# Performance work log

Measured on AMD Instinct MI355X. Metric: run time of the kernel, lower is better.

Reference implementation:

```python
import jax, jax.numpy as jnp
import numpy as np

H = 8      # heads
D = 64     # dim_head
N0 = 1024  # modality-0 tokens
N1 = 1024  # modality-1 tokens
N = N0 + N1  # == token_num
DI = H * D   # dim_inner = 512


def setup_inputs() -> dict:
    key = jax.random.key(0)
    ks = jax.random.split(key, 10)
    s = 0.02
    return {
        "x0": jax.random.normal(ks[0], (1, N0, 512), jnp.float32),
        "x1": jax.random.normal(ks[1], (1, N1, 512), jnp.float32),
        "mask0": jnp.ones((1, N0), jnp.bool_),
        "mask1": jnp.ones((1, N1), jnp.bool_),
        "attn_dist": jax.random.normal(ks[2], (1, N, N), jnp.float32),
        "W_in0": jax.random.normal(ks[3], (512, 3 * DI), jnp.float32) * s,
        "W_in1": jax.random.normal(ks[4], (512, 3 * DI), jnp.float32) * s,
        "W_tau": jax.random.normal(ks[5], (DI, N * H), jnp.float32) * s,
        "b_tau": jax.random.normal(ks[6], (N * H,), jnp.float32) * s,
        "W_out0": jax.random.normal(ks[7], (DI, 512), jnp.float32) * s,
        "W_out1": jax.random.normal(ks[8], (DI, 512), jnp.float32) * s,
    }


def _split_heads(qkv, B, n):
    # (B, n, 3*H*D) -> (3, B, H, n, D)   [matches Rearrange 'b n (qkv h d) -> qkv b h n d']
    return qkv.reshape(B, n, 3, H, D).transpose(2, 0, 3, 1, 4)


def reference(x0, x1, mask0, mask1, attn_dist, W_in0, W_in1, W_tau, b_tau, W_out0, W_out1):
    B = x0.shape[0]
    qkv0 = _split_heads(x0 @ W_in0, B, N0)
    qkv1 = _split_heads(x1 @ W_in1, B, N1)
    qkv = jnp.concatenate([qkv0, qkv1], axis=3)  # pack along token axis -> (3,B,H,N,D)
    q, k, v = qkv[0], qkv[1], qkv[2]
    mask = jnp.concatenate([mask0, mask1], axis=1)  # (B, N)

    sim = jnp.einsum('bhid,bhjd->bhij', q, k) / jnp.sqrt(jnp.array(D, q.dtype))
    neg = -jnp.finfo(sim.dtype).max
    sim = jnp.where(mask[:, None, None, :], sim, neg)

    # taus: raw row-major reshape of q (B,H,N,D) -> (B,N,H*D), as in torch .reshape
    q_flat = q.reshape(B, N, H * D)
    taus = (q_flat @ W_tau + b_tau).reshape(B, N, N, H)
    bias = (taus * attn_dist[..., None]).transpose(0, 3, 1, 2)  # (B,H,N,N)
    sim = sim - bias

    attn = jax.nn.softmax(sim.astype(jnp.float32), axis=-1).astype(sim.dtype)
    out = jnp.einsum('bhij,bhjd->bhid', attn, v)
    out = out.transpose(0, 2, 1, 3).reshape(B, N, H * D)  # merge heads

    out0 = out[:, :N0] @ W_out0
    out1 = out[:, N0:] @ W_out1
    return (out0, out1)
```

## Files before the change

kernel.cpp:

```cpp
#include <hip/hip_runtime.h>
#include <stdint.h>

typedef __bf16 bf16;
typedef __bf16 bf16x8 __attribute__((ext_vector_type(8)));
typedef float f32x4 __attribute__((ext_vector_type(4)));
typedef unsigned short u16x8 __attribute__((ext_vector_type(8)));

#define MFMA16(a, b, c) __builtin_amdgcn_mfma_f32_16x16x32_bf16(a, b, c, 0, 0, 0)

static __device__ __forceinline__ bf16x8 lds_frag(const unsigned short* p) {
  return __builtin_bit_cast(bf16x8, *(const u16x8*)p);
}

static __device__ __forceinline__ u16x8 cvt8(const float* p) {
  f32x4 a = *(const f32x4*)p;
  f32x4 b = *(const f32x4*)(p + 4);
  u16x8 r;
#pragma unroll
  for (int e = 0; e < 4; ++e) {
    r[e] = __builtin_bit_cast(unsigned short, (bf16)a[e]);
    r[4 + e] = __builtin_bit_cast(unsigned short, (bf16)b[e]);
  }
  return r;
}

__global__ __launch_bounds__(256) void wtau_transpose(
    const float* __restrict__ Wti, const float* __restrict__ btau,
    bf16* __restrict__ Wto, float* __restrict__ bto) {
  const int c0 = blockIdx.x * 64;
  const int j0 = blockIdx.y * 32;
  const int tid = threadIdx.x;
  __shared__ unsigned short tile[8 * 32 * 72];

#pragma unroll
  for (int it = 0; it < 8; ++it) {
    int idx = it * 256 + tid;
    int c = idx >> 5, j = idx & 31;
    u16x8 v = cvt8(Wti + (size_t)(c0 + c) * 16384 + (j0 + j) * 8);
#pragma unroll
    for (int h = 0; h < 8; ++h) tile[(h * 32 + j) * 72 + c] = v[h];
  }
  __syncthreads();
#pragma unroll
  for (int it = 0; it < 8; ++it) {
    int chunk = it * 256 + tid;
    int row = chunk >> 3, ck = chunk & 7;
    int h = row >> 5, j = row & 31;
    u16x8 v = *(const u16x8*)&tile[row * 72 + ck * 8];
    *(u16x8*)((unsigned short*)Wto + (size_t)(h * 2048 + j0 + j) * 512 + c0 + ck * 8) = v;
  }
  if (blockIdx.x == 0) {
    int idx = tid;
    int j = idx >> 3, h = idx & 7;
    bto[h * 2048 + j0 + j] = btau[(j0 + j) * 8 + h];
  }
}

__global__ __launch_bounds__(256) void qkv_gemm(
    const float* __restrict__ x0, const float* __restrict__ x1,
    const float* __restrict__ Win0, const float* __restrict__ Win1,
    bf16* __restrict__ Qb, bf16* __restrict__ Kb, bf16* __restrict__ Vb) {
  const int mod = blockIdx.z;
  const float* Am = mod ? x1 : x0;
  const float* Bm = mod ? Win1 : Win0;
  const int i0 = blockIdx.x * 64;
  const int c0 = blockIdx.y * 64;
  const int tid = threadIdx.x;
  const int lane = tid & 63, wave = tid >> 6;
  const int l16 = lane & 15, quad = lane >> 4;
  const int mrow = (wave & 1) * 32, ncol = (wave >> 1) * 32;
  __shared__ unsigned short As[64 * 32];
  __shared__ unsigned short Bs[64 * 32];
  f32x4 acc[2][2] = {};

  const int arow = tid >> 2, akc = tid & 3;
  const int bkr = tid >> 3, bnc = tid & 7;
  for (int k0 = 0; k0 < 512; k0 += 32) {
    u16x8 va = cvt8(Am + (size_t)(i0 + arow) * 512 + k0 + akc * 8);
    u16x8 vb = cvt8(Bm + (size_t)(k0 + bkr) * 1536 + c0 + bnc * 8);
    __syncthreads();
    *(u16x8*)&As[arow * 32 + akc * 8] = va;
#pragma unroll
    for (int e = 0; e < 8; ++e) Bs[(bnc * 8 + e) * 32 + bkr] = vb[e];
    __syncthreads();
    bf16x8 a[2], b[2];
#pragma unroll
    for (int mt = 0; mt < 2; ++mt) a[mt] = lds_frag(&As[(mrow + mt * 16 + l16) * 32 + quad * 8]);
#pragma unroll
    for (int nt = 0; nt < 2; ++nt) b[nt] = lds_frag(&Bs[(ncol + nt * 16 + l16) * 32 + quad * 8]);
#pragma unroll
    for (int mt = 0; mt < 2; ++mt)
#pragma unroll
      for (int nt = 0; nt < 2; ++nt) acc[mt][nt] = MFMA16(a[mt], b[nt], acc[mt][nt]);
  }
#pragma unroll
  for (int mt = 0; mt < 2; ++mt)
#pragma unroll
    for (int nt = 0; nt < 2; ++nt)
#pragma unroll
      for (int r = 0; r < 4; ++r) {
        int row = i0 + mrow + mt * 16 + quad * 4 + r;
        int col = c0 + ncol + nt * 16 + l16;
        int qsel = col >> 9, h = (col >> 6) & 7, d = col & 63;
        bf16* dst = qsel == 0 ? Qb : (qsel == 1 ? Kb : Vb);
        dst[(size_t)(h * 2048 + mod * 1024 + row) * 64 + d] = (bf16)acc[mt][nt][r];
      }
}

__global__ __launch_bounds__(256) void tau_gemm(
    const bf16* __restrict__ Qb, const bf16* __restrict__ Wt,
    const float* __restrict__ bt, const float* __restrict__ ad, bf16* __restrict__ T) {
  const int h = blockIdx.z;
  const int i0 = blockIdx.x * 128, j0 = blockIdx.y * 128;
  const bf16* Bm = Wt + (size_t)h * (2048 * 512);
  const int tid = threadIdx.x;
  const int lane = tid & 63, wave = tid >> 6;
  const int l16 = lane & 15, quad = lane >> 4;
  const int mrow = (wave & 1) * 64, ncol = (wave >> 1) * 64;
  __shared__ unsigned short As[128 * 64];
  __shared__ unsigned short Bs[128 * 64];
  f32x4 acc[4][4] = {};

  for (int k0 = 0; k0 < 512; k0 += 64) {
    __syncthreads();
#pragma unroll
    for (int c = 0; c < 4; ++c) {
      int s = c * 256 + tid;
      int row = s >> 3, pos = s & 7;
      int kc = pos ^ (row & 7);
      __builtin_amdgcn_global_load_lds((const unsigned int*)(Qb + (size_t)(i0 + row) * 512 + k0 + kc * 8),
                                       (unsigned int*)&As[s * 8], 16, 0, 0);
      __builtin_amdgcn_global_load_lds((const unsigned int*)(Bm + (size_t)(j0 + row) * 512 + k0 + kc * 8),
                                       (unsigned int*)&Bs[s * 8], 16, 0, 0);
    }
    __syncthreads();
#pragma unroll
    for (int kb = 0; kb < 2; ++kb) {
      bf16x8 a[4], b[4];
#pragma unroll
      for (int mt = 0; mt < 4; ++mt) {
        int row = mrow + mt * 16 + l16;
        a[mt] = lds_frag(&As[row * 64 + (((kb * 4 + quad) ^ (row & 7)) * 8)]);
      }
#pragma unroll
      for (int nt = 0; nt < 4; ++nt) {
        int row = ncol + nt * 16 + l16;
        b[nt] = lds_frag(&Bs[row * 64 + (((kb * 4 + quad) ^ (row & 7)) * 8)]);
      }
#pragma unroll
      for (int mt = 0; mt < 4; ++mt)
#pragma unroll
        for (int nt = 0; nt < 4; ++nt) acc[mt][nt] = MFMA16(a[mt], b[nt], acc[mt][nt]);
    }
  }
  float btv[4];
#pragma unroll
  for (int nt = 0; nt < 4; ++nt) btv[nt] = bt[h * 2048 + j0 + ncol + nt * 16 + l16];
  bf16* Th = T + (size_t)h * (2048 * 2048);
#pragma unroll
  for (int mt = 0; mt < 4; ++mt)
#pragma unroll
    for (int nt = 0; nt < 4; ++nt)
#pragma unroll
      for (int r = 0; r < 4; ++r) {
        int row = i0 + mrow + mt * 16 + quad * 4 + r;
        int col = j0 + ncol + nt * 16 + l16;
        float av = ad[(size_t)row * 2048 + col];
        Th[(size_t)row * 2048 + col] = (bf16)((acc[mt][nt][r] + btv[nt]) * av);
      }
}

__global__ __launch_bounds__(256) void attn_kernel(
    const bf16* __restrict__ Qb, const bf16* __restrict__ Kb, const bf16* __restrict__ Vb,
    const bf16* __restrict__ T, float* __restrict__ Op, float* __restrict__ Ml) {
  const int h = blockIdx.y;
  const int i0 = blockIdx.x * 64;
  const int js = blockIdx.z;
  const int tid = threadIdx.x;
  const int lane = tid & 63, wave = tid >> 6;
  const int l16 = lane & 15, quad = lane >> 4;
  __shared__ unsigned short Ks[64 * 72];
  __shared__ unsigned short Vt[64 * 72];
  __shared__ unsigned short Ps[64 * 72];
  __shared__ unsigned short Tb[64 * 64];

  bf16x8 aQ[2];
#pragma unroll
  for (int kk = 0; kk < 2; ++kk)
    aQ[kk] = __builtin_bit_cast(
        bf16x8, *(const u16x8*)((const unsigned short*)Qb +
                                (size_t)(h * 2048 + i0 + wave * 16 + l16) * 64 + kk * 32 + quad * 8));
  f32x4 Oacc[4] = {};
  float m_run[4], l_run[4];
#pragma unroll
  for (int r = 0; r < 4; ++r) { m_run[r] = -3.0e38f; l_run[r] = 0.f; }
  const bf16* Th = T + (size_t)h * (2048 * 2048);

  for (int t = 0; t < 8; ++t) {
    const int j0 = js * 512 + t * 64;
    u16x8 vk[2], vv[2];
#pragma unroll
    for (int c = 0; c < 2; ++c) {
      int s = c * 256 + tid;
      int row = s >> 3, dc = s & 7;
      vk[c] = *(const u16x8*)((const unsigned short*)Kb + (size_t)(h * 2048 + j0 + row) * 64 + dc * 8);
      vv[c] = *(const u16x8*)((const unsigned short*)Vb + (size_t)(h * 2048 + j0 + row) * 64 + dc * 8);
    }
    __syncthreads();
#pragma unroll
    for (int c = 0; c < 2; ++c) {
      int s = c * 256 + tid;
      __builtin_amdgcn_global_load_lds(
          (const unsigned int*)(Th + (size_t)(i0 + (s >> 3)) * 2048 + j0 + (s & 7) * 8),
          (unsigned int*)&Tb[s * 8], 16, 0, 0);
      int row = s >> 3, dc = s & 7;
      *(u16x8*)&Ks[row * 72 + dc * 8] = vk[c];
#pragma unroll
      for (int e = 0; e < 8; ++e) Vt[(dc * 8 + e) * 72 + row] = vv[c][e];
    }
    __syncthreads();

    f32x4 S[4] = {};
#pragma unroll
    for (int nt = 0; nt < 4; ++nt)
#pragma unroll
      for (int kk = 0; kk < 2; ++kk) {
        bf16x8 bk = lds_frag(&Ks[(nt * 16 + l16) * 72 + kk * 32 + quad * 8]);
        S[nt] = MFMA16(aQ[kk], bk, S[nt]);
      }
    float sv[4][4];
#pragma unroll
    for (int nt = 0; nt < 4; ++nt)
#pragma unroll
      for (int r = 0; r < 4; ++r) {
        float tb = (float)__builtin_bit_cast(
            bf16, Tb[(wave * 16 + quad * 4 + r) * 64 + nt * 16 + l16]);
        sv[nt][r] = S[nt][r] * 0.125f - tb;
      }
#pragma unroll
    for (int r = 0; r < 4; ++r) {
      float mx = fmaxf(fmaxf(sv[0][r], sv[1][r]), fmaxf(sv[2][r], sv[3][r]));
#pragma unroll
      for (int o = 1; o < 16; o <<= 1) mx = fmaxf(mx, __shfl_xor(mx, o, 16));
      float mnew = fmaxf(m_run[r], mx);
      float alpha = __expf(m_run[r] - mnew);
      m_run[r] = mnew;
      float rs = 0.f;
#pragma unroll
      for (int nt = 0; nt < 4; ++nt) { sv[nt][r] = __expf(sv[nt][r] - mnew); rs += sv[nt][r]; }
#pragma unroll
      for (int o = 1; o < 16; o <<= 1) rs += __shfl_xor(rs, o, 16);
      l_run[r] = l_run[r] * alpha + rs;
#pragma unroll
      for (int dt = 0; dt < 4; ++dt) Oacc[dt][r] *= alpha;
    }
#pragma unroll
    for (int nt = 0; nt < 4; ++nt)
#pragma unroll
      for (int r = 0; r < 4; ++r)
        Ps[(wave * 16 + quad * 4 + r) * 72 + nt * 16 + l16] =
            __builtin_bit_cast(unsigned short, (bf16)sv[nt][r]);
    __syncthreads();
#pragma unroll
    for (int kk = 0; kk < 2; ++kk) {
      bf16x8 aP = lds_frag(&Ps[(wave * 16 + l16) * 72 + kk * 32 + quad * 8]);
#pragma unroll
      for (int dt = 0; dt < 4; ++dt) {
        bf16x8 bv = lds_frag(&Vt[(dt * 16 + l16) * 72 + kk * 32 + quad * 8]);
        Oacc[dt] = MFMA16(aP, bv, Oacc[dt]);
      }
    }
  }
  const size_t pb = ((size_t)js * 8 + h) * 2048;
#pragma unroll
  for (int r = 0; r < 4; ++r) {
    int rowg = i0 + wave * 16 + quad * 4 + r;
#pragma unroll
    for (int dt = 0; dt < 4; ++dt)
      Op[(pb + rowg) * 64 + dt * 16 + l16] = Oacc[dt][r];
    if (l16 == 0) {
      Ml[(pb + rowg) * 2 + 0] = m_run[r];
      Ml[(pb + rowg) * 2 + 1] = l_run[r];
    }
  }
}

__global__ __launch_bounds__(256) void merge_kernel(
    const float* __restrict__ Op, const float* __restrict__ Ml, bf16* __restrict__ om) {
  const int gr = blockIdx.x * 4 + (threadIdx.x >> 6);
  const int d = threadIdx.x & 63;
  float ms[4];
  float mmax = -3.0e38f;
#pragma unroll
  for (int s = 0; s < 4; ++s) {
    ms[s] = Ml[((size_t)s * 16384 + gr) * 2 + 0];
    mmax = fmaxf(mmax, ms[s]);
  }
  float lsum = 0.f, o = 0.f;
#pragma unroll
  for (int s = 0; s < 4; ++s) {
    float w = __expf(ms[s] - mmax);
    lsum += Ml[((size_t)s * 16384 + gr) * 2 + 1] * w;
    o += Op[((size_t)s * 16384 + gr) * 64 + d] * w;
  }
  int h = gr >> 11, i = gr & 2047;
  om[(size_t)i * 512 + h * 64 + d] = (bf16)(o / lsum);
}

__global__ __launch_bounds__(256) void out_proj(
    const bf16* __restrict__ om, const float* __restrict__ Wo0, const float* __restrict__ Wo1,
    float* __restrict__ out) {
  const int mod = blockIdx.z;
  const bf16* Am = om + (size_t)mod * (1024 * 512);
  const float* Bm = mod ? Wo1 : Wo0;
  float* outp = out + (size_t)mod * (1024 * 512);
  const int i0 = blockIdx.x * 64;
  const int c0 = blockIdx.y * 64;
  const int tid = threadIdx.x;
  const int lane = tid & 63, wave = tid >> 6;
  const int l16 = lane & 15, quad = lane >> 4;
  const int mrow = (wave & 1) * 32, ncol = (wave >> 1) * 32;
  __shared__ unsigned short As[64 * 32];
  __shared__ unsigned short Bs[64 * 32];
  f32x4 acc[2][2] = {};

  const int arow = tid >> 2, akc = tid & 3;
  const int bkr = tid >> 3, bnc = tid & 7;
  for (int k0 = 0; k0 < 512; k0 += 32) {
    u16x8 va = *(const u16x8*)((const unsigned short*)Am + (size_t)(i0 + arow) * 512 + k0 + akc * 8);
    u16x8 vb = cvt8(Bm + (size_t)(k0 + bkr) * 512 + c0 + bnc * 8);
    __syncthreads();
    *(u16x8*)&As[arow * 32 + akc * 8] = va;
#pragma unroll
    for (int e = 0; e < 8; ++e) Bs[(bnc * 8 + e) * 32 + bkr] = vb[e];
    __syncthreads();
    bf16x8 a[2], b[2];
#pragma unroll
    for (int mt = 0; mt < 2; ++mt) a[mt] = lds_frag(&As[(mrow + mt * 16 + l16) * 32 + quad * 8]);
#pragma unroll
    for (int nt = 0; nt < 2; ++nt) b[nt] = lds_frag(&Bs[(ncol + nt * 16 + l16) * 32 + quad * 8]);
#pragma unroll
    for (int mt = 0; mt < 2; ++mt)
#pragma unroll
      for (int nt = 0; nt < 2; ++nt) acc[mt][nt] = MFMA16(a[mt], b[nt], acc[mt][nt]);
  }
#pragma unroll
  for (int mt = 0; mt < 2; ++mt)
#pragma unroll
    for (int nt = 0; nt < 2; ++nt)
#pragma unroll
      for (int r = 0; r < 4; ++r) {
        int row = i0 + mrow + mt * 16 + quad * 4 + r;
        int col = c0 + ncol + nt * 16 + l16;
        outp[(size_t)row * 512 + col] = acc[mt][nt][r];
      }
}

extern "C" void kernel_launch(void* const* d_in, const int* in_sizes, int n_in,
                              void* d_out, int out_size, void* d_ws, size_t ws_size,
                              hipStream_t stream) {
  (void)in_sizes; (void)n_in; (void)out_size; (void)ws_size;
  const float* x0   = (const float*)d_in[0];
  const float* x1   = (const float*)d_in[1];
  const float* ad   = (const float*)d_in[4];
  const float* Win0 = (const float*)d_in[5];
  const float* Win1 = (const float*)d_in[6];
  const float* Wtau = (const float*)d_in[7];
  const float* btau = (const float*)d_in[8];
  const float* Wo0  = (const float*)d_in[9];
  const float* Wo1  = (const float*)d_in[10];
  float* out = (float*)d_out;

  bf16* ws = (bf16*)d_ws;
  bf16* Qb = ws;
  bf16* Kb = Qb + 1048576;
  bf16* Vb = Kb + 1048576;
  bf16* Wt = Vb + 1048576;
  bf16* T  = Wt + 8388608;
  bf16* om = T + 33554432;
  float* bt = (float*)(om + 1048576);
  float* Ml = bt + 16384;
  float* Op = (float*)Wt;

  wtau_transpose<<<dim3(8, 64), 256, 0, stream>>>(Wtau, btau, Wt, bt);
  qkv_gemm<<<dim3(16, 24, 2), 256, 0, stream>>>(x0, x1, Win0, Win1, Qb, Kb, Vb);
  tau_gemm<<<dim3(16, 16, 8), 256, 0, stream>>>(Qb, Wt, bt, ad, T);
  attn_kernel<<<dim3(32, 8, 4), 256, 0, stream>>>(Qb, Kb, Vb, T, Op, Ml);
  merge_kernel<<<4096, 256, 0, stream>>>(Op, Ml, om);
  out_proj<<<dim3(16, 8, 2), 256, 0, stream>>>(om, Wo0, Wo1, out);
}
```

Baseline: 265.2 us.

## Pre-convert inputs and weights to bf16 in one prep kernel, use direct LDS loads

```diff
diff --git a/kernel.cpp b/kernel.cpp
--- a/kernel.cpp
+++ b/kernel.cpp
@@ -24,86 +24,153 @@
   return r;
 }
 
-__global__ __launch_bounds__(256) void wtau_transpose(
+__global__ __launch_bounds__(256) void prep_kernel(
     const float* __restrict__ Wti, const float* __restrict__ btau,
-    bf16* __restrict__ Wto, float* __restrict__ bto) {
-  const int c0 = blockIdx.x * 64;
-  const int j0 = blockIdx.y * 32;
-  const int tid = threadIdx.x;
-  __shared__ unsigned short tile[8 * 32 * 72];
-
-#pragma unroll
-  for (int it = 0; it < 8; ++it) {
-    int idx = it * 256 + tid;
-    int c = idx >> 5, j = idx & 31;
-    u16x8 v = cvt8(Wti + (size_t)(c0 + c) * 16384 + (j0 + j) * 8);
-#pragma unroll
-    for (int h = 0; h < 8; ++h) tile[(h * 32 + j) * 72 + c] = v[h];
-  }
-  __syncthreads();
-#pragma unroll
-  for (int it = 0; it < 8; ++it) {
-    int chunk = it * 256 + tid;
-    int row = chunk >> 3, ck = chunk & 7;
-    int h = row >> 5, j = row & 31;
-    u16x8 v = *(const u16x8*)&tile[row * 72 + ck * 8];
-    *(u16x8*)((unsigned short*)Wto + (size_t)(h * 2048 + j0 + j) * 512 + c0 + ck * 8) = v;
-  }
-  if (blockIdx.x == 0) {
-    int idx = tid;
-    int j = idx >> 3, h = idx & 7;
-    bto[h * 2048 + j0 + j] = btau[(j0 + j) * 8 + h];
-  }
-}
-
-__global__ __launch_bounds__(256) void qkv_gemm(
     const float* __restrict__ x0, const float* __restrict__ x1,
     const float* __restrict__ Win0, const float* __restrict__ Win1,
+    const float* __restrict__ Wo0, const float* __restrict__ Wo1,
+    bf16* __restrict__ Wto, float* __restrict__ bto, bf16* __restrict__ xb,
+    bf16* __restrict__ Winb0, bf16* __restrict__ Winb1,
+    bf16* __restrict__ Wob0, bf16* __restrict__ Wob1) {
+  const int b = blockIdx.x;
+  const int tid = threadIdx.x;
+  __shared__ unsigned short shm[8 * 32 * 72];
+
+  if (b < 512) {
+    const int c0 = (b & 7) * 64;
+    const int j0 = (b >> 3) * 32;
+#pragma unroll
+    for (int it = 0; it < 8; ++it) {
+      int idx = it * 256 + tid;
+      int c = idx >> 5, j = idx & 31;
+      u16x8 v = cvt8(Wti + (size_t)(c0 + c) * 16384 + (j0 + j) * 8);
+#pragma unroll
+      for (int h = 0; h < 8; ++h) shm[(h * 32 + j) * 72 + c] = v[h];
+    }
+    __syncthreads();
+#pragma unroll
+    for (int it = 0; it < 8; ++it) {
+      int chunk = it * 256 + tid;
+      int row = chunk >> 3, ck = chunk & 7;
+      int h = row >> 5, j = row & 31;
+      u16x8 v = *(const u16x8*)&shm[row * 72 + ck * 8];
+      *(u16x8*)((unsigned short*)Wto + (size_t)(h * 2048 + j0 + j) * 512 + c0 + ck * 8) = v;
+    }
+    if ((b & 7) == 0) {
+      int j = tid >> 3, h = tid & 7;
+      bto[h * 2048 + j0 + j] = btau[(j0 + j) * 8 + h];
+    }
+  } else if (b < 896) {
+    int t = b - 512;
+    const float* W = t < 192 ? Win0 : Win1;
+    bf16* Wb = t < 192 ? Winb0 : Winb1;
+    t = t < 192 ? t : t - 192;
+    const int c0 = (t & 7) * 64, n0 = (t >> 3) * 64;
+#pragma unroll
+    for (int it = 0; it < 2; ++it) {
+      int idx = it * 256 + tid;
+      int c = idx >> 3, nn = idx & 7;
+      u16x8 v = cvt8(W + (size_t)(c0 + c) * 1536 + n0 + nn * 8);
+#pragma unroll
+      for (int e = 0; e < 8; ++e) shm[(nn * 8 + e) * 72 + c] = v[e];
+    }
+    __syncthreads();
+#pragma unroll
+    for (int it = 0; it < 2; ++it) {
+      int idx = it * 256 + tid;
+      int n = idx >> 3, ck = idx & 7;
+      *(u16x8*)((unsigned short*)Wb + (size_t)(n0 + n) * 512 + c0 + ck * 8) =
+          *(const u16x8*)&shm[n * 72 + ck * 8];
+    }
+  } else if (b < 1408) {
+    int t = b - 896;
+    const float* src = t < 256 ? x0 : x1;
+    size_t dst0 = t < 256 ? 0 : 524288;
+    int tt = t < 256 ? t : t - 256;
+    size_t off = (size_t)tt * 2048 + tid * 8;
+    u16x8 v = cvt8(src + off);
+    *(u16x8*)((unsigned short*)xb + dst0 + off) = v;
+  } else {
+    int t = b - 1408;
+    const float* W = t < 64 ? Wo0 : Wo1;
+    bf16* Wb = t < 64 ? Wob0 : Wob1;
+    t &= 63;
+    const int c0 = (t & 7) * 64, n0 = (t >> 3) * 64;
+#pragma unroll
+    for (int it = 0; it < 2; ++it) {
+      int idx = it * 256 + tid;
+      int c = idx >> 3, nn = idx & 7;
+      u16x8 v = cvt8(W + (size_t)(c0 + c) * 512 + n0 + nn * 8);
+#pragma unroll
+      for (int e = 0; e < 8; ++e) shm[(nn * 8 + e) * 72 + c] = v[e];
+    }
+    __syncthreads();
+#pragma unroll
+    for (int it = 0; it < 2; ++it) {
+      int idx = it * 256 + tid;
+      int n = idx >> 3, ck = idx & 7;
+      *(u16x8*)((unsigned short*)Wb + (size_t)(n0 + n) * 512 + c0 + ck * 8) =
+          *(const u16x8*)&shm[n * 72 + ck * 8];
+    }
+  }
+}
+
+__global__ __launch_bounds__(256) void qkv_gemm(
+    const bf16* __restrict__ xb, const bf16* __restrict__ Winb0, const bf16* __restrict__ Winb1,
     bf16* __restrict__ Qb, bf16* __restrict__ Kb, bf16* __restrict__ Vb) {
-  const int mod = blockIdx.z;
-  const float* Am = mod ? x1 : x0;
-  const float* Bm = mod ? Win1 : Win0;
-  const int i0 = blockIdx.x * 64;
-  const int c0 = blockIdx.y * 64;
+  const int i0 = blockIdx.x * 128, c0 = blockIdx.y * 128;
+  const bf16* Bm = (i0 < 1024) ? Winb0 : Winb1;
   const int tid = threadIdx.x;
   const int lane = tid & 63, wave = tid >> 6;
   const int l16 = lane & 15, quad = lane >> 4;
-  const int mrow = (wave & 1) * 32, ncol = (wave >> 1) * 32;
-  __shared__ unsigned short As[64 * 32];
-  __shared__ unsigned short Bs[64 * 32];
-  f32x4 acc[2][2] = {};
-
-  const int arow = tid >> 2, akc = tid & 3;
-  const int bkr = tid >> 3, bnc = tid & 7;
-  for (int k0 = 0; k0 < 512; k0 += 32) {
-    u16x8 va = cvt8(Am + (size_t)(i0 + arow) * 512 + k0 + akc * 8);
-    u16x8 vb = cvt8(Bm + (size_t)(k0 + bkr) * 1536 + c0 + bnc * 8);
-    __syncthreads();
-    *(u16x8*)&As[arow * 32 + akc * 8] = va;
-#pragma unroll
-    for (int e = 0; e < 8; ++e) Bs[(bnc * 8 + e) * 32 + bkr] = vb[e];
-    __syncthreads();
-    bf16x8 a[2], b[2];
-#pragma unroll
-    for (int mt = 0; mt < 2; ++mt) a[mt] = lds_frag(&As[(mrow + mt * 16 + l16) * 32 + quad * 8]);
-#pragma unroll
-    for (int nt = 0; nt < 2; ++nt) b[nt] = lds_frag(&Bs[(ncol + nt * 16 + l16) * 32 + quad * 8]);
-#pragma unroll
-    for (int mt = 0; mt < 2; ++mt)
-#pragma unroll
-      for (int nt = 0; nt < 2; ++nt) acc[mt][nt] = MFMA16(a[mt], b[nt], acc[mt][nt]);
-  }
-#pragma unroll
-  for (int mt = 0; mt < 2; ++mt)
-#pragma unroll
-    for (int nt = 0; nt < 2; ++nt)
+  const int mrow = (wave & 1) * 64, ncol = (wave >> 1) * 64;
+  __shared__ unsigned short As[128 * 64];
+  __shared__ unsigned short Bs[128 * 64];
+  f32x4 acc[4][4] = {};
+
+  for (int k0 = 0; k0 < 512; k0 += 64) {
+    __syncthreads();
+#pragma unroll
+    for (int c = 0; c < 4; ++c) {
+      int s = c * 256 + tid;
+      int row = s >> 3, pos = s & 7;
+      int kc = pos ^ (row & 7);
+      __builtin_amdgcn_global_load_lds((const unsigned int*)(xb + (size_t)(i0 + row) * 512 + k0 + kc * 8),
+                                       (unsigned int*)&As[s * 8], 16, 0, 0);
+      __builtin_amdgcn_global_load_lds((const unsigned int*)(Bm + (size_t)(c0 + row) * 512 + k0 + kc * 8),
+                                       (unsigned int*)&Bs[s * 8], 16, 0, 0);
+    }
+    __syncthreads();
+#pragma unroll
+    for (int kb = 0; kb < 2; ++kb) {
+      bf16x8 a[4], b[4];
+#pragma unroll
+      for (int mt = 0; mt < 4; ++mt) {
+        int row = mrow + mt * 16 + l16;
+        a[mt] = lds_frag(&As[row * 64 + (((kb * 4 + quad) ^ (row & 7)) * 8)]);
+      }
+#pragma unroll
+      for (int nt = 0; nt < 4; ++nt) {
+        int row = ncol + nt * 16 + l16;
+        b[nt] = lds_frag(&Bs[row * 64 + (((kb * 4 + quad) ^ (row & 7)) * 8)]);
+      }
+#pragma unroll
+      for (int mt = 0; mt < 4; ++mt)
+#pragma unroll
+        for (int nt = 0; nt < 4; ++nt) acc[mt][nt] = MFMA16(a[mt], b[nt], acc[mt][nt]);
+    }
+  }
+#pragma unroll
+  for (int mt = 0; mt < 4; ++mt)
+#pragma unroll
+    for (int nt = 0; nt < 4; ++nt)
 #pragma unroll
       for (int r = 0; r < 4; ++r) {
         int row = i0 + mrow + mt * 16 + quad * 4 + r;
         int col = c0 + ncol + nt * 16 + l16;
         int qsel = col >> 9, h = (col >> 6) & 7, d = col & 63;
         bf16* dst = qsel == 0 ? Qb : (qsel == 1 ? Kb : Vb);
-        dst[(size_t)(h * 2048 + mod * 1024 + row) * 64 + d] = (bf16)acc[mt][nt][r];
+        dst[(size_t)(h * 2048 + row) * 64 + d] = (bf16)acc[mt][nt][r];
       }
 }
 
@@ -308,41 +375,52 @@
 }
 
 __global__ __launch_bounds__(256) void out_proj(
-    const bf16* __restrict__ om, const float* __restrict__ Wo0, const float* __restrict__ Wo1,
+    const bf16* __restrict__ om, const bf16* __restrict__ Wob0, const bf16* __restrict__ Wob1,
     float* __restrict__ out) {
   const int mod = blockIdx.z;
-  const bf16* Am = om + (size_t)mod * (1024 * 512);
-  const float* Bm = mod ? Wo1 : Wo0;
+  const bf16* Bw = mod ? Wob1 : Wob0;
   float* outp = out + (size_t)mod * (1024 * 512);
-  const int i0 = blockIdx.x * 64;
-  const int c0 = blockIdx.y * 64;
+  const int i0 = blockIdx.x * 64, c0 = blockIdx.y * 64;
+  const int grow0 = mod * 1024 + i0;
   const int tid = threadIdx.x;
   const int lane = tid & 63, wave = tid >> 6;
   const int l16 = lane & 15, quad = lane >> 4;
   const int mrow = (wave & 1) * 32, ncol = (wave >> 1) * 32;
-  __shared__ unsigned short As[64 * 32];
-  __shared__ unsigned short Bs[64 * 32];
+  __shared__ unsigned short As[64 * 64];
+  __shared__ unsigned short Bs[64 * 64];
   f32x4 acc[2][2] = {};
 
-  const int arow = tid >> 2, akc = tid & 3;
-  const int bkr = tid >> 3, bnc = tid & 7;
-  for (int k0 = 0; k0 < 512; k0 += 32) {
-    u16x8 va = *(const u16x8*)((const unsigned short*)Am + (size_t)(i0 + arow) * 512 + k0 + akc * 8);
-    u16x8 vb = cvt8(Bm + (size_t)(k0 + bkr) * 512 + c0 + bnc * 8);
-    __syncthreads();
-    *(u16x8*)&As[arow * 32 + akc * 8] = va;
-#pragma unroll
-    for (int e = 0; e < 8; ++e) Bs[(bnc * 8 + e) * 32 + bkr] = vb[e];
-    __syncthreads();
-    bf16x8 a[2], b[2];
-#pragma unroll
-    for (int mt = 0; mt < 2; ++mt) a[mt] = lds_frag(&As[(mrow + mt * 16 + l16) * 32 + quad * 8]);
-#pragma unroll
-    for (int nt = 0; nt < 2; ++nt) b[nt] = lds_frag(&Bs[(ncol + nt * 16 + l16) * 32 + quad * 8]);
-#pragma unroll
-    for (int mt = 0; mt < 2; ++mt)
-#pragma unroll
-      for (int nt = 0; nt < 2; ++nt) acc[mt][nt] = MFMA16(a[mt], b[nt], acc[mt][nt]);
+  for (int k0 = 0; k0 < 512; k0 += 64) {
+    __syncthreads();
+#pragma unroll
+    for (int c = 0; c < 2; ++c) {
+      int s = c * 256 + tid;
+      int row = s >> 3, pos = s & 7;
+      int kc = pos ^ (row & 7);
+      __builtin_amdgcn_global_load_lds((const unsigned int*)(om + (size_t)(grow0 + row) * 512 + k0 + kc * 8),
+                                       (unsigned int*)&As[s * 8], 16, 0, 0);
+      __builtin_amdgcn_global_load_lds((const unsigned int*)(Bw + (size_t)(c0 + row) * 512 + k0 + kc * 8),
+                                       (unsigned int*)&Bs[s * 8], 16, 0, 0);
+    }
+    __syncthreads();
+#pragma unroll
+    for (int kb = 0; kb < 2; ++kb) {
+      bf16x8 a[2], b[2];
+#pragma unroll
+      for (int mt = 0; mt < 2; ++mt) {
+        int row = mrow + mt * 16 + l16;
+        a[mt] = lds_frag(&As[row * 64 + (((kb * 4 + quad) ^ (row & 7)) * 8)]);
+      }
+#pragma unroll
+      for (int nt = 0; nt < 2; ++nt) {
+        int row = ncol + nt * 16 + l16;
+        b[nt] = lds_frag(&Bs[row * 64 + (((kb * 4 + quad) ^ (row & 7)) * 8)]);
+      }
+#pragma unroll
+      for (int mt = 0; mt < 2; ++mt)
+#pragma unroll
+        for (int nt = 0; nt < 2; ++nt) acc[mt][nt] = MFMA16(a[mt], b[nt], acc[mt][nt]);
+    }
   }
 #pragma unroll
   for (int mt = 0; mt < 2; ++mt)
@@ -380,12 +458,18 @@
   bf16* om = T + 33554432;
   float* bt = (float*)(om + 1048576);
   float* Ml = bt + 16384;
+  bf16* Wob0 = (bf16*)(Ml + 131072);
+  bf16* Wob1 = Wob0 + 262144;
   float* Op = (float*)Wt;
-
-  wtau_transpose<<<dim3(8, 64), 256, 0, stream>>>(Wtau, btau, Wt, bt);
-  qkv_gemm<<<dim3(16, 24, 2), 256, 0, stream>>>(x0, x1, Win0, Win1, Qb, Kb, Vb);
+  bf16* xb    = T;
+  bf16* Winb0 = T + 1048576;
+  bf16* Winb1 = Winb0 + 786432;
+
+  prep_kernel<<<1536, 256, 0, stream>>>(Wtau, btau, x0, x1, Win0, Win1, Wo0, Wo1,
+                                        Wt, bt, xb, Winb0, Winb1, Wob0, Wob1);
+  qkv_gemm<<<dim3(16, 12), 256, 0, stream>>>(xb, Winb0, Winb1, Qb, Kb, Vb);
   tau_gemm<<<dim3(16, 16, 8), 256, 0, stream>>>(Qb, Wt, bt, ad, T);
   attn_kernel<<<dim3(32, 8, 4), 256, 0, stream>>>(Qb, Kb, Vb, T, Op, Ml);
   merge_kernel<<<4096, 256, 0, stream>>>(Op, Ml, om);
-  out_proj<<<dim3(16, 8, 2), 256, 0, stream>>>(om, Wo0, Wo1, out);
-}
+  out_proj<<<dim3(16, 8, 2), 256, 0, stream>>>(om, Wob0, Wob1, out);
+}
```

Measured after the change: 243.1 us. -8.3%, faster.
